# Performance work log

Hardware: AMD Instinct MI355X
Metric: run time of the kernel (lower is better)

Reference implementation:

```python
import jax, jax.numpy as jnp
import numpy as np

# 8 fixed 3x3 shift-and-subtract kernels (center -1, one neighbor +1)
_KERNELS = np.array([
    [[1, 0, 0], [0, -1, 0], [0, 0, 0]],
    [[0, 1, 0], [0, -1, 0], [0, 0, 0]],
    [[0, 0, 1], [0, -1, 0], [0, 0, 0]],
    [[0, 0, 0], [1, -1, 0], [0, 0, 0]],
    [[0, 0, 0], [0, -1, 1], [0, 0, 0]],
    [[0, 0, 0], [0, -1, 0], [1, 0, 0]],
    [[0, 0, 0], [0, -1, 0], [0, 1, 0]],
    [[0, 0, 0], [0, -1, 0], [0, 0, 1]],
], dtype=np.float32)  # [8,3,3]


def contrast_depth_conv(x):
    # x: [B, H, W] single-channel depth map.
    # torch does groups=8 depthwise conv on the input broadcast to 8 channels,
    # which is identical to a 1->8 channel VALID conv with the 8 kernels.
    w = jnp.asarray(_KERNELS)[:, None, :, :]  # [8,1,3,3] OIHW
    y = jax.lax.conv_general_dilated(
        x[:, None, :, :],  # [B,1,H,W] NCHW
        w,
        window_strides=(1, 1),
        padding='VALID',
        dimension_numbers=('NCHW', 'OIHW', 'NCHW'),
    )
    return y  # [B, 8, H-2, W-2]


def setup_inputs() -> dict:
    key = jax.random.key(0)
    k1, k2 = jax.random.split(key)
    B, H, W = 16384, 32, 32
    out = jax.random.normal(k1, (B, H, W), dtype=jnp.float32)
    label = jax.random.normal(k2, (B, H, W), dtype=jnp.float32)
    return {"out": out, "label": label}


def reference(out, label):
    c_out = contrast_depth_conv(out)      # [B,8,30,30]
    c_label = contrast_depth_conv(label)  # [B,8,30,30]
    diff = c_out - c_label
    return jnp.mean(diff * diff)
```

## Files before the change

kernel.cpp:

```cpp
#include <hip/hip_runtime.h>


#define THREADS 256

__global__ __launch_bounds__(THREADS) void cdl_partial(
    const float* __restrict__ outp,
    const float* __restrict__ labp,
    float* __restrict__ partial,
    int nimg)
{
    const int t    = threadIdx.x;
    const int lane = t & 63;
    const int wid  = t >> 6;
    const int img  = blockIdx.x * 4 + wid;

    float acc = 0.f;

    if (img < nimg) {
        const float* ob = outp + img * 1024;
        const float* lb = labp + img * 1024;

        #pragma unroll
        for (int i = 0; i < 4; ++i) {
            const int task = i * 64 + lane;
            if (task < 225) {
                const int qy = task / 15;
                const int qx = task - qy * 15;
                const int y = 2 * qy + 1;
                const int x = 2 * qx + 1;
                const int base = (y - 1) * 32 + (x - 1);

                float dd[4][4];
                #pragma unroll
                for (int r = 0; r < 4; ++r) {
                    const float2 o0 = *(const float2*)(ob + base + r * 32);
                    const float2 o1 = *(const float2*)(ob + base + r * 32 + 2);
                    const float2 l0 = *(const float2*)(lb + base + r * 32);
                    const float2 l1 = *(const float2*)(lb + base + r * 32 + 2);
                    dd[r][0] = o0.x - l0.x;
                    dd[r][1] = o0.y - l0.y;
                    dd[r][2] = o1.x - l1.x;
                    dd[r][3] = o1.y - l1.y;
                }

                #pragma unroll
                for (int cy = 0; cy < 2; ++cy) {
                    #pragma unroll
                    for (int cx = 0; cx < 2; ++cx) {
                        const float c = dd[cy + 1][cx + 1];
                        #pragma unroll
                        for (int ny = 0; ny < 3; ++ny) {
                            #pragma unroll
                            for (int nx = 0; nx < 3; ++nx) {
                                if (ny == 1 && nx == 1) continue;
                                const float v = dd[cy + ny][cx + nx] - c;
                                acc += v * v;
                            }
                        }
                    }
                }
            }
        }
    }

    #pragma unroll
    for (int off = 32; off; off >>= 1) acc += __shfl_down(acc, off, 64);
    __shared__ float red[4];
    if (lane == 0) red[wid] = acc;
    __syncthreads();
    if (t == 0) partial[blockIdx.x] = red[0] + red[1] + red[2] + red[3];
}

__global__ __launch_bounds__(THREADS) void cdl_final(
    const float* __restrict__ partial,
    float* __restrict__ out,
    int np,
    float inv_count)
{
    __shared__ float red[THREADS / 64];
    const int t = threadIdx.x;
    float acc = 0.f;
    for (int i = t; i < np; i += THREADS) acc += partial[i];
    #pragma unroll
    for (int off = 32; off; off >>= 1) acc += __shfl_down(acc, off, 64);
    if ((t & 63) == 0) red[t >> 6] = acc;
    __syncthreads();
    if (t == 0) out[0] = (red[0] + red[1] + red[2] + red[3]) * inv_count;
}

extern "C" void kernel_launch(void* const* d_in, const int* in_sizes, int n_in,
                              void* d_out, int out_size, void* d_ws, size_t ws_size,
                              hipStream_t stream) {
    const float* outp = (const float*)d_in[0];
    const float* labp = (const float*)d_in[1];
    float* partial = (float*)d_ws;
    const int nimg = in_sizes[0] / 1024;
    const int nblocks = (nimg + 3) / 4;
    const float inv_count = 1.0f / ((float)nimg * 8.0f * 900.0f);

    cdl_partial<<<nblocks, THREADS, 0, stream>>>(outp, labp, partial, nimg);
    cdl_final<<<1, THREADS, 0, stream>>>(partial, (float*)d_out, nblocks, inv_count);
}
```

Baseline: 30.61 us.

## Stage image differences in LDS with coalesced float4 loads and double buffering

Each block now handles 8 images in turn. All 256 threads load each image with coalesced float4 reads, write the out-label difference into a padded, double-buffered shared-memory tile, and the first 225 threads compute the 2x2-patch stencil from LDS. The next image's loads are issued before the current image is processed, so global latency overlaps with compute. This replaces the earlier overlapping float2 global reads, which fetched each element several times. The cost is one block barrier per image and fewer, larger blocks.

```diff
diff --git a/kernel.cpp b/kernel.cpp
--- a/kernel.cpp
+++ b/kernel.cpp
@@ -2,70 +2,77 @@
 
 
 #define THREADS 256
+#define IPB 8
+#define STRIDE 36
 
-__global__ __launch_bounds__(THREADS) void cdl_partial(
+__global__ __launch_bounds__(THREADS, 8) void cdl_partial(
     const float* __restrict__ outp,
     const float* __restrict__ labp,
     float* __restrict__ partial,
     int nimg)
 {
-    const int t    = threadIdx.x;
-    const int lane = t & 63;
-    const int wid  = t >> 6;
-    const int img  = blockIdx.x * 4 + wid;
+    __shared__ float d[2][32][STRIDE];
+    const int t   = threadIdx.x;
+    const int row = t >> 3;
+    const int col = (t & 7) << 2;
+
+    const int b0 = blockIdx.x * IPB;
+    const float4* op = (const float4*)outp + (long long)b0 * 256 + t;
+    const float4* lp = (const float4*)labp + (long long)b0 * 256 + t;
+
+    const bool active = t < 225;
+    const int qy = t / 15, qx = t - qy * 15;
+    const int ry = 2 * qy, cx = 2 * qx;
 
     float acc = 0.f;
 
-    if (img < nimg) {
-        const float* ob = outp + img * 1024;
-        const float* lb = labp + img * 1024;
+    float4 o = *op, l = *lp;
+    float4 dv = make_float4(o.x - l.x, o.y - l.y, o.z - l.z, o.w - l.w);
 
-        #pragma unroll
-        for (int i = 0; i < 4; ++i) {
-            const int task = i * 64 + lane;
-            if (task < 225) {
-                const int qy = task / 15;
-                const int qx = task - qy * 15;
-                const int y = 2 * qy + 1;
-                const int x = 2 * qx + 1;
-                const int base = (y - 1) * 32 + (x - 1);
+    const int n = (nimg - b0 < IPB) ? (nimg - b0) : IPB;
+    for (int i = 0; i < n; ++i) {
+        float4 on, ln;
+        const bool more = (i + 1 < n);
+        if (more) { on = op[(i + 1) * 256]; ln = lp[(i + 1) * 256]; }
 
-                float dd[4][4];
+        *(float4*)&d[i & 1][row][col] = dv;
+        __syncthreads();
+
+        if (active) {
+            const float (*im)[STRIDE] = d[i & 1];
+            float dd[4][4];
+            #pragma unroll
+            for (int r = 0; r < 4; ++r) {
+                const float2 a = *(const float2*)&im[ry + r][cx];
+                const float2 b = *(const float2*)&im[ry + r][cx + 2];
+                dd[r][0] = a.x; dd[r][1] = a.y; dd[r][2] = b.x; dd[r][3] = b.y;
+            }
+            #pragma unroll
+            for (int cyy = 0; cyy < 2; ++cyy) {
                 #pragma unroll
-                for (int r = 0; r < 4; ++r) {
-                    const float2 o0 = *(const float2*)(ob + base + r * 32);
-                    const float2 o1 = *(const float2*)(ob + base + r * 32 + 2);
-                    const float2 l0 = *(const float2*)(lb + base + r * 32);
-                    const float2 l1 = *(const float2*)(lb + base + r * 32 + 2);
-                    dd[r][0] = o0.x - l0.x;
-                    dd[r][1] = o0.y - l0.y;
-                    dd[r][2] = o1.x - l1.x;
-                    dd[r][3] = o1.y - l1.y;
-                }
-
-                #pragma unroll
-                for (int cy = 0; cy < 2; ++cy) {
+                for (int cxx = 0; cxx < 2; ++cxx) {
+                    const float c = dd[cyy + 1][cxx + 1];
                     #pragma unroll
-                    for (int cx = 0; cx < 2; ++cx) {
-                        const float c = dd[cy + 1][cx + 1];
+                    for (int ny = 0; ny < 3; ++ny) {
                         #pragma unroll
-                        for (int ny = 0; ny < 3; ++ny) {
-                            #pragma unroll
-                            for (int nx = 0; nx < 3; ++nx) {
-                                if (ny == 1 && nx == 1) continue;
-                                const float v = dd[cy + ny][cx + nx] - c;
-                                acc += v * v;
-                            }
+                        for (int nx = 0; nx < 3; ++nx) {
+                            if (ny == 1 && nx == 1) continue;
+                            const float v = dd[cyy + ny][cxx + nx] - c;
+                            acc += v * v;
                         }
                     }
                 }
             }
         }
+
+        if (more)
+            dv = make_float4(on.x - ln.x, on.y - ln.y, on.z - ln.z, on.w - ln.w);
     }
 
     #pragma unroll
     for (int off = 32; off; off >>= 1) acc += __shfl_down(acc, off, 64);
     __shared__ float red[4];
+    const int lane = t & 63, wid = t >> 6;
     if (lane == 0) red[wid] = acc;
     __syncthreads();
     if (t == 0) partial[blockIdx.x] = red[0] + red[1] + red[2] + red[3];
@@ -95,7 +102,7 @@
     const float* labp = (const float*)d_in[1];
     float* partial = (float*)d_ws;
     const int nimg = in_sizes[0] / 1024;
-    const int nblocks = (nimg + 3) / 4;
+    const int nblocks = (nimg + IPB - 1) / IPB;
     const float inv_count = 1.0f / ((float)nimg * 8.0f * 900.0f);
 
     cdl_partial<<<nblocks, THREADS, 0, stream>>>(outp, labp, partial, nimg);
```

New measurement: 29.39 us. 4.0% less time.

## Use coalesced float4 row loads with wave shuffles and fuse final reduction

Applied to the files above, without the earlier changes.

Each wave now processes two images. Every lane loads one float4 per row group in a fully coalesced pattern, and lanes exchange neighbor differences through cross-lane shuffles instead of re-reading overlapping float2 windows from global memory. The separate final-reduction kernel is replaced by a last-block-done pattern that uses an atomic counter, which needs an extra memset per launch. The aim is to cut redundant global loads and one kernel launch, at the cost of many shuffles per element and masking arithmetic for border lanes and rows.

```diff
diff --git a/kernel.cpp b/kernel.cpp
--- a/kernel.cpp
+++ b/kernel.cpp
@@ -3,62 +3,75 @@
 
 #define THREADS 256
 
-__global__ __launch_bounds__(THREADS) void cdl_partial(
+__global__ __launch_bounds__(THREADS, 8) void cdl_fused(
     const float* __restrict__ outp,
     const float* __restrict__ labp,
     float* __restrict__ partial,
-    int nimg)
+    int* __restrict__ counter,
+    float* __restrict__ out,
+    int nimg, float inv_count)
 {
     const int t    = threadIdx.x;
     const int lane = t & 63;
     const int wid  = t >> 6;
-    const int img  = blockIdx.x * 4 + wid;
+    const int img0 = (blockIdx.x * 4 + wid) * 2;
+
+    const int cg = lane & 7;
+    const int r  = lane >> 3;
+    const float w0   = (cg == 0) ? 0.f : 1.f;
+    const float w3   = (cg == 7) ? 0.f : 1.f;
+    const float mrow = (r >= 1 && r <= 6) ? 1.f : 0.f;
 
     float acc = 0.f;
 
-    if (img < nimg) {
-        const float* ob = outp + img * 1024;
-        const float* lb = labp + img * 1024;
+    const float4* ob = (const float4*)outp + (long long)img0 * 256 + lane;
+    const float4* lb = (const float4*)labp + (long long)img0 * 256 + lane;
 
-        #pragma unroll
-        for (int i = 0; i < 4; ++i) {
-            const int task = i * 64 + lane;
-            if (task < 225) {
-                const int qy = task / 15;
-                const int qx = task - qy * 15;
-                const int y = 2 * qy + 1;
-                const int x = 2 * qx + 1;
-                const int base = (y - 1) * 32 + (x - 1);
+    #pragma unroll
+    for (int im = 0; im < 2; ++im) {
+        if (img0 + im < nimg) {
+            const float4* obase = ob + im * 256;
+            const float4* lbase = lb + im * 256;
+            #pragma unroll
+            for (int s2 = 0; s2 < 5; ++s2) {
+                const float4 o = obase[s2 * 48];
+                const float4 l = lbase[s2 * 48];
+                const float d0 = o.x - l.x, d1 = o.y - l.y,
+                            d2 = o.z - l.z, d3 = o.w - l.w;
+                const float u0 = __shfl(d0, lane - 8), u1 = __shfl(d1, lane - 8),
+                            u2 = __shfl(d2, lane - 8), u3 = __shfl(d3, lane - 8);
+                const float v0 = __shfl(d0, lane + 8), v1 = __shfl(d1, lane + 8),
+                            v2 = __shfl(d2, lane + 8), v3 = __shfl(d3, lane + 8);
+                const float dL = __shfl(d3, lane - 1), dR = __shfl(d0, lane + 1);
+                const float uL = __shfl(d3, lane - 9), uR = __shfl(d0, lane - 7);
+                const float vL = __shfl(d3, lane + 7), vR = __shfl(d0, lane + 9);
+                float s, vv, tot;
+                s = 0.f;
+                vv = uL - d0; s += vv * vv;  vv = u0 - d0; s += vv * vv;
+                vv = u1 - d0; s += vv * vv;  vv = dL - d0; s += vv * vv;
+                vv = d1 - d0; s += vv * vv;  vv = vL - d0; s += vv * vv;
+                vv = v0 - d0; s += vv * vv;  vv = v1 - d0; s += vv * vv;
+                tot = w0 * s;
+                s = 0.f;
+                vv = u0 - d1; s += vv * vv;  vv = u1 - d1; s += vv * vv;
+                vv = u2 - d1; s += vv * vv;  vv = d0 - d1; s += vv * vv;
+                vv = d2 - d1; s += vv * vv;  vv = v0 - d1; s += vv * vv;
+                vv = v1 - d1; s += vv * vv;  vv = v2 - d1; s += vv * vv;
+                tot += s;
+                s = 0.f;
+                vv = u1 - d2; s += vv * vv;  vv = u2 - d2; s += vv * vv;
+                vv = u3 - d2; s += vv * vv;  vv = d1 - d2; s += vv * vv;
+                vv = d3 - d2; s += vv * vv;  vv = v1 - d2; s += vv * vv;
+                vv = v2 - d2; s += vv * vv;  vv = v3 - d2; s += vv * vv;
+                tot += s;
+                s = 0.f;
+                vv = u2 - d3; s += vv * vv;  vv = u3 - d3; s += vv * vv;
+                vv = uR - d3; s += vv * vv;  vv = d2 - d3; s += vv * vv;
+                vv = dR - d3; s += vv * vv;  vv = v2 - d3; s += vv * vv;
+                vv = v3 - d3; s += vv * vv;  vv = vR - d3; s += vv * vv;
+                tot += w3 * s;
 
-                float dd[4][4];
-                #pragma unroll
-                for (int r = 0; r < 4; ++r) {
-                    const float2 o0 = *(const float2*)(ob + base + r * 32);
-                    const float2 o1 = *(const float2*)(ob + base + r * 32 + 2);
-                    const float2 l0 = *(const float2*)(lb + base + r * 32);
-                    const float2 l1 = *(const float2*)(lb + base + r * 32 + 2);
-                    dd[r][0] = o0.x - l0.x;
-                    dd[r][1] = o0.y - l0.y;
-                    dd[r][2] = o1.x - l1.x;
-                    dd[r][3] = o1.y - l1.y;
-                }
-
-                #pragma unroll
-                for (int cy = 0; cy < 2; ++cy) {
-                    #pragma unroll
-                    for (int cx = 0; cx < 2; ++cx) {
-                        const float c = dd[cy + 1][cx + 1];
-                        #pragma unroll
-                        for (int ny = 0; ny < 3; ++ny) {
-                            #pragma unroll
-                            for (int nx = 0; nx < 3; ++nx) {
-                                if (ny == 1 && nx == 1) continue;
-                                const float v = dd[cy + ny][cx + nx] - c;
-                                acc += v * v;
-                            }
-                        }
-                    }
-                }
+                acc += mrow * tot;
             }
         }
     }
@@ -68,24 +81,25 @@
     __shared__ float red[4];
     if (lane == 0) red[wid] = acc;
     __syncthreads();
-    if (t == 0) partial[blockIdx.x] = red[0] + red[1] + red[2] + red[3];
-}
+    if (t == 0) {
+        partial[blockIdx.x] = red[0] + red[1] + red[2] + red[3];
+        __threadfence();
+    }
+    __syncthreads();
 
-__global__ __launch_bounds__(THREADS) void cdl_final(
-    const float* __restrict__ partial,
-    float* __restrict__ out,
-    int np,
-    float inv_count)
-{
-    __shared__ float red[THREADS / 64];
-    const int t = threadIdx.x;
-    float acc = 0.f;
-    for (int i = t; i < np; i += THREADS) acc += partial[i];
-    #pragma unroll
-    for (int off = 32; off; off >>= 1) acc += __shfl_down(acc, off, 64);
-    if ((t & 63) == 0) red[t >> 6] = acc;
+    __shared__ int is_last;
+    if (t == 0) is_last = (atomicAdd(counter, 1) == (int)gridDim.x - 1) ? 1 : 0;
     __syncthreads();
-    if (t == 0) out[0] = (red[0] + red[1] + red[2] + red[3]) * inv_count;
+    if (is_last) {
+        __threadfence();
+        float a = 0.f;
+        for (int i = t; i < (int)gridDim.x; i += THREADS) a += partial[i];
+        #pragma unroll
+        for (int off = 32; off; off >>= 1) a += __shfl_down(a, off, 64);
+        if (lane == 0) red[wid] = a;
+        __syncthreads();
+        if (t == 0) out[0] = (red[0] + red[1] + red[2] + red[3]) * inv_count;
+    }
 }
 
 extern "C" void kernel_launch(void* const* d_in, const int* in_sizes, int n_in,
@@ -93,11 +107,14 @@
                               hipStream_t stream) {
     const float* outp = (const float*)d_in[0];
     const float* labp = (const float*)d_in[1];
-    float* partial = (float*)d_ws;
     const int nimg = in_sizes[0] / 1024;
-    const int nblocks = (nimg + 3) / 4;
+    const int nblocks = (nimg + 7) / 8;
     const float inv_count = 1.0f / ((float)nimg * 8.0f * 900.0f);
 
-    cdl_partial<<<nblocks, THREADS, 0, stream>>>(outp, labp, partial, nimg);
-    cdl_final<<<1, THREADS, 0, stream>>>(partial, (float*)d_out, nblocks, inv_count);
+    int* counter = (int*)d_ws;
+    float* partial = (float*)d_ws + 64;
+    hipMemsetAsync(counter, 0, sizeof(int), stream);
+
+    cdl_fused<<<nblocks, THREADS, 0, stream>>>(outp, labp, partial, counter,
+                                               (float*)d_out, nimg, inv_count);
 }
```

Measured after the change: 98.62 us. +222.2%, slower.
